# Optimization experiments

Hardware: AMD Instinct MI355X
Metric: run time of the kernel (lower is better)

Reference implementation:

```python
import jax, jax.numpy as jnp
import numpy as np

# dims
B_, L_, DM = 2, 2048, 2048
DS, DC, EXP, HD, NG, CH = 128, 4, 2, 64, 1, 256
DI = EXP * DM                    # d_inner = d_ssm = 4096
NH = DI // HD                    # 64 heads
DIP = 2 * DI + 2 * NG * DS + NH  # 8448 in_proj output
CDIM = DI + 2 * NG * DS          # 4352 conv channels
EPS = 1e-5


def setup_inputs() -> dict:
    key = jax.random.key(0)
    ks = jax.random.split(key, 6)
    u = jax.random.normal(ks[0], (B_, L_, DM), jnp.float32)
    w_in = jax.random.normal(ks[1], (DM, DIP), jnp.float32) * 0.02
    conv_w = jax.random.normal(ks[2], (CDIM, DC), jnp.float32) * (1.0 / np.sqrt(DC))
    conv_b = jnp.zeros((CDIM,), jnp.float32)
    # dt_bias init exactly as the torch module (dt_min=1e-3, dt_max=0.1)
    dt = jnp.exp(jax.random.uniform(ks[3], (NH,)) * (np.log(0.1) - np.log(0.001)) + np.log(0.001))
    dt = jnp.clip(dt, 1e-4)
    dt_bias = dt + jnp.log(-jnp.expm1(-dt))
    A_log = jnp.log(jax.random.uniform(ks[4], (NH,), minval=1.0, maxval=16.0))
    D_skip = jnp.ones((NH,), jnp.float32)
    norm_w = jnp.ones((DI,), jnp.float32)
    return dict(u=u, w_in=w_in, conv_w=conv_w, conv_b=conv_b,
                dt_bias=dt_bias, A_log=A_log, D_skip=D_skip, norm_w=norm_w)


def _segsum(x):
    # x: (..., T) -> (..., T, T) lower-triangular segment sums, -inf above diag
    T = x.shape[-1]
    cs = jnp.cumsum(x, -1)
    ss = cs[..., :, None] - cs[..., None, :]
    return jnp.where(jnp.tril(jnp.ones((T, T), bool)), ss, -jnp.inf)


def _ssd(xdt, dA, Bm, Cm):
    # xdt: (b,l,h,p) = x*dt, dA: (b,l,h) = dt*A, Bm/Cm: (b,l,g,n)
    b, l, h, p = xdt.shape
    c = l // CH
    xr = xdt.reshape(b, c, CH, h, p)
    dAr = dA.reshape(b, c, CH, h).transpose(0, 3, 1, 2)        # (b,h,c,t)
    rep = h // NG
    Bh = jnp.repeat(Bm.reshape(b, c, CH, NG, DS), rep, axis=3)  # (b,c,t,h,n)
    Ch = jnp.repeat(Cm.reshape(b, c, CH, NG, DS), rep, axis=3)
    Acs = jnp.cumsum(dAr, -1)                                   # (b,h,c,t)
    Lm = jnp.exp(_segsum(dAr))                                  # (b,h,c,t,t)
    # intra-chunk (diagonal block) output
    Yd = jnp.einsum('bcthn,bcshn,bhcts,bcshp->bcthp', Ch, Bh, Lm, xr)
    # per-chunk final states
    decay_st = jnp.exp(Acs[..., -1:] - Acs)                     # (b,h,c,t)
    states = jnp.einsum('bcthn,bhct,bcthp->bchpn', Bh, decay_st, xr)
    # inter-chunk recurrence
    pad_last = jnp.pad(Acs[..., -1], ((0, 0), (0, 0), (1, 0)))  # (b,h,c+1)
    dchunk = jnp.exp(_segsum(pad_last))                         # (b,h,c+1,c+1)
    states = jnp.concatenate([jnp.zeros_like(states[:, :1]), states], 1)
    init_st = jnp.einsum('bhzc,bchpn->bzhpn', dchunk, states)[:, :-1]  # (b,c,h,p,n)
    Yo = jnp.einsum('bcthn,bchpn,bhct->bcthp', Ch, init_st, jnp.exp(Acs))
    return (Yd + Yo).reshape(b, l, h, p)


def reference(u, w_in, conv_w, conv_b, dt_bias, A_log, D_skip, norm_w):
    zxbcdt = u @ w_in                           # (b,l,8448)
    z = zxbcdt[..., :DI]
    xBC = zxbcdt[..., DI:DI + CDIM]
    dt = zxbcdt[..., DI + CDIM:]                # (b,l,nheads)
    # causal depthwise conv1d (kernel DC, left pad DC-1) + SiLU
    xp = jnp.pad(xBC, ((0, 0), (DC - 1, 0), (0, 0)))
    xBC = sum(xp[:, k:k + L_, :] * conv_w[:, k] for k in range(DC)) + conv_b
    xBC = jax.nn.silu(xBC)
    x = xBC[..., :DI].reshape(B_, L_, NH, HD)
    Bm = xBC[..., DI:DI + NG * DS].reshape(B_, L_, NG, DS)
    Cm = xBC[..., DI + NG * DS:].reshape(B_, L_, NG, DS)
    dt = jax.nn.softplus(dt + dt_bias)          # dt_softplus=True
    A = -jnp.exp(A_log)
    y = _ssd(x * dt[..., None], dt * A, Bm, Cm)
    y = y + x * D_skip[None, None, :, None]     # D skip, per-head
    y = y.reshape(B_, L_, DI)
    # gated RMSNorm, norm_before_gate=False: rmsnorm(y * silu(z)) * weight
    yg = y * jax.nn.silu(z)
    return yg * jax.lax.rsqrt(jnp.mean(yg * yg, -1, keepdims=True) + EPS) * norm_w
```

## Files before the change

kernel.cpp:

```cpp
#include <hip/hip_runtime.h>
#include <hip/hip_bf16.h>

#define B_SZ   2
#define L_SZ   2048
#define DM     2048
#define DS     128
#define DCV    4
#define HD     64
#define CH     256
#define DI     4096
#define NH     64
#define DIP    8512
#define CDIM   4352
#define NP     8576
#define MROWS  4096
#define NCK    8

typedef __attribute__((ext_vector_type(8))) short bf16x8;
typedef __attribute__((ext_vector_type(4))) float f32x4;
typedef unsigned short u16;

__device__ __forceinline__ u16 f2bf(float f) {
    union { float f; unsigned u; } c; c.f = f;
    unsigned r = c.u + 0x7fffu + ((c.u >> 16) & 1u);
    return (u16)(r >> 16);
}
__device__ __forceinline__ float bf2f(u16 b) {
    union { unsigned u; float f; } c; c.u = ((unsigned)b) << 16; return c.f;
}

__device__ __forceinline__ void async16(const u16* g, u16* l) {
    __builtin_amdgcn_global_load_lds(
        (const __attribute__((address_space(1))) unsigned int*)(g),
        (__attribute__((address_space(3))) unsigned int*)(l),
        16, 0, 0);
}

__global__ void cvt_u_kernel(const float* __restrict__ u, u16* __restrict__ ub) {
    int i = blockIdx.x * 256 + threadIdx.x;
    float4 v = ((const float4*)u)[i];
    ushort4 o;
    o.x = f2bf(v.x); o.y = f2bf(v.y); o.z = f2bf(v.z); o.w = f2bf(v.w);
    ((ushort4*)ub)[i] = o;
}

__global__ void transpose_w_kernel(const float* __restrict__ w, u16* __restrict__ wt) {
    __shared__ float tile[32][33];
    int n0 = blockIdx.x * 32, k0 = blockIdx.y * 32;
    int tx = threadIdx.x & 31, ty = threadIdx.x >> 5;
    for (int j = 0; j < 32; j += 8) {
        int k = k0 + ty + j, n = n0 + tx;
        tile[ty + j][tx] = (n < DIP) ? w[(size_t)k * DIP + n] : 0.f;
    }
    __syncthreads();
    for (int j = 0; j < 32; j += 8) {
        int n = n0 + ty + j, k = k0 + tx;
        wt[(size_t)n * DM + k] = f2bf(tile[tx][ty + j]);
    }
}

#define G_NKT   32
#define G_NBLK  1072
__global__ __launch_bounds__(512) void gemm_kernel(const u16* __restrict__ A,
                                                   const u16* __restrict__ Bt,
                                                   u16* __restrict__ C) {
    __shared__ u16 As[3][256 * 64];
    __shared__ u16 Bs[3][128 * 64];

    int bid = blockIdx.x;
    int bidx = (bid & 7) * (G_NBLK / 8) + (bid >> 3);
    const int width = 8 * 67;
    int group = bidx / width;
    int rem = bidx - group * width;
    int pid_m = group * 8 + (rem & 7);
    int pid_n = rem >> 3;
    const int m0 = pid_m * 256, n0 = pid_n * 128;

    const int tid = threadIdx.x;
    const int lane = tid & 63, wid = tid >> 6;
    const int wm = (wid >> 1) * 64;
    const int wn = (wid & 1) * 64;
    const int quad = lane >> 4, lm = lane & 15;
    const int sx = lm & 7;

    const int srow = tid >> 3;
    const int sc8 = (tid & 7) ^ (srow & 7);
    const u16* aS = A  + (size_t)(m0 + srow) * DM + sc8 * 8;
    const u16* bS = Bt + (size_t)(n0 + srow) * DM + sc8 * 8;
    const int ldo = srow * 64 + (tid & 7) * 8;

    f32x4 acc[4][4] = {};

    for (int t = 0; t < 2; t++) {
        const u16* as = aS + t * 64;
        const u16* bs = bS + t * 64;
        for (int q = 0; q < 4; q++) async16(as + (size_t)q * 64 * DM, &As[t][ldo + q * 4096]);
        for (int q = 0; q < 2; q++) async16(bs + (size_t)q * 64 * DM, &Bs[t][ldo + q * 4096]);
    }
    asm volatile("s_waitcnt vmcnt(6)" ::: "memory");
    __builtin_amdgcn_s_barrier();

    for (int kt = 0; kt < G_NKT; kt++) {
        unsigned cur = (unsigned)kt % 3u;
        unsigned sb  = (unsigned)(kt + 2) % 3u;
        const bool dost = (kt + 2) < G_NKT;
        const u16* ab = &As[cur][0];
        const u16* bb = &Bs[cur][0];
        const u16* as = aS + (kt + 2) * 64;
        const u16* bs = bS + (kt + 2) * 64;

        bf16x8 af[4][2], bf0[2][2];
        for (int i = 0; i < 4; i++) {
            int row = wm + i * 16 + lm;
            for (int ks = 0; ks < 2; ks++)
                af[i][ks] = *(const bf16x8*)(ab + row * 64 + (((ks * 4 + quad) ^ sx) * 8));
        }
        for (int j = 0; j < 2; j++) {
            int row = wn + j * 16 + lm;
            for (int ks = 0; ks < 2; ks++)
                bf0[j][ks] = *(const bf16x8*)(bb + row * 64 + (((ks * 4 + quad) ^ sx) * 8));
        }
        if (dost) {
            async16(as,                   &As[sb][ldo]);
            async16(as + (size_t)64 * DM, &As[sb][ldo + 4096]);
            async16(bs,                   &Bs[sb][ldo]);
        }
        __builtin_amdgcn_s_barrier();
        asm volatile("s_waitcnt lgkmcnt(0)" ::: "memory");
        __builtin_amdgcn_s_setprio(1);
        for (int ks = 0; ks < 2; ks++)
            for (int i = 0; i < 4; i++)
                for (int j = 0; j < 2; j++)
                    acc[i][j] = __builtin_amdgcn_mfma_f32_16x16x32_bf16(af[i][ks], bf0[j][ks], acc[i][j], 0, 0, 0);
        __builtin_amdgcn_s_setprio(0);
        __builtin_amdgcn_s_barrier();

        bf16x8 bf1[2][2];
        for (int j = 0; j < 2; j++) {
            int row = wn + (j + 2) * 16 + lm;
            for (int ks = 0; ks < 2; ks++)
                bf1[j][ks] = *(const bf16x8*)(bb + row * 64 + (((ks * 4 + quad) ^ sx) * 8));
        }
        if (dost) {
            async16(as + (size_t)128 * DM, &As[sb][ldo + 8192]);
            async16(as + (size_t)192 * DM, &As[sb][ldo + 12288]);
            async16(bs + (size_t)64 * DM,  &Bs[sb][ldo + 4096]);
        }
        if (kt < G_NKT - 2) { asm volatile("s_waitcnt vmcnt(6)" ::: "memory"); }
        else                { asm volatile("s_waitcnt vmcnt(0)" ::: "memory"); }
        __builtin_amdgcn_s_barrier();
        asm volatile("s_waitcnt lgkmcnt(0)" ::: "memory");
        __builtin_amdgcn_s_setprio(1);
        for (int ks = 0; ks < 2; ks++)
            for (int i = 0; i < 4; i++)
                for (int j = 0; j < 2; j++)
                    acc[i][j + 2] = __builtin_amdgcn_mfma_f32_16x16x32_bf16(af[i][ks], bf1[j][ks], acc[i][j + 2], 0, 0, 0);
        __builtin_amdgcn_s_setprio(0);
        __builtin_amdgcn_s_barrier();
    }

    for (int i = 0; i < 4; i++)
        for (int j = 0; j < 4; j++)
            for (int r = 0; r < 4; r++) {
                int gm = m0 + wm + i * 16 + quad * 4 + r;
                int gn = n0 + wn + j * 16 + lm;
                C[(size_t)gm * NP + gn] = f2bf(acc[i][j][r]);
            }
}

__global__ void conv_silu_kernel(const u16* __restrict__ zx, const float* __restrict__ cw,
                                 const float* __restrict__ cb, u16* __restrict__ xbc) {
    int c = blockIdx.x * 256 + threadIdx.x;
    int row = blockIdx.y;
    int l = row & (L_SZ - 1);
    float acc = cb[c];
    for (int k = 0; k < DCV; k++) {
        int ls = l - 3 + k;
        if (ls >= 0) acc += bf2f(zx[(size_t)(row - 3 + k) * NP + DI + c]) * cw[c * DCV + k];
    }
    float s = acc / (1.f + expf(-acc));
    xbc[(size_t)row * CDIM + c] = f2bf(s);
}

__global__ void dt_scan_kernel(const u16* __restrict__ zx, const float* __restrict__ dt_bias,
                               const float* __restrict__ A_log, float* __restrict__ dtbT,
                               float* __restrict__ acs) {
    int bid = blockIdx.x;
    int h = bid & 63, c = (bid >> 6) & 7, b = bid >> 9;
    int t = threadIdx.x;
    int row = b * L_SZ + c * CH + t;
    float raw = bf2f(zx[(size_t)row * NP + (DI + CDIM) + h]) + dt_bias[h];
    float dtv = (raw > 20.f) ? raw : log1pf(expf(raw));
    float dA = dtv * (-expf(A_log[h]));
    dtbT[(size_t)h * MROWS + row] = dtv;
    __shared__ float sc[256];
    sc[t] = dA;
    for (int off = 1; off < 256; off <<= 1) {
        __syncthreads();
        float v = (t >= off) ? sc[t - off] : 0.f;
        __syncthreads();
        sc[t] += v;
    }
    acs[((size_t)((b * NH + h) * NCK + c)) * CH + t] = sc[t];
}

__global__ void g_kernel(const u16* __restrict__ xbc, u16* __restrict__ Gb) {
    int blk = blockIdx.x;
    int bc = blk >> 4;
    int tile = blk & 15;
    int tb0 = (tile >> 2) * 64, sb0 = (tile & 3) * 64;
    int row0 = bc * CH;
    __shared__ float Ct[64][65], Bt_[64][65];
    int tq = (threadIdx.x >> 4) * 4;
    int sq = (threadIdx.x & 15) * 4;
    float acc[4][4] = {};
    for (int nh = 0; nh < 2; nh++) {
        __syncthreads();
        int r = threadIdx.x >> 2, cc = (threadIdx.x & 3) * 16;
        for (int q = 0; q < 16; q += 4) {
            ushort4 cv = *(const ushort4*)&xbc[(size_t)(row0 + tb0 + r) * CDIM + (DI + DS) + nh * 64 + cc + q];
            ushort4 bv = *(const ushort4*)&xbc[(size_t)(row0 + sb0 + r) * CDIM + DI + nh * 64 + cc + q];
            Ct[r][cc + q] = bf2f(cv.x); Ct[r][cc + q + 1] = bf2f(cv.y); Ct[r][cc + q + 2] = bf2f(cv.z); Ct[r][cc + q + 3] = bf2f(cv.w);
            Bt_[r][cc + q] = bf2f(bv.x); Bt_[r][cc + q + 1] = bf2f(bv.y); Bt_[r][cc + q + 2] = bf2f(bv.z); Bt_[r][cc + q + 3] = bf2f(bv.w);
        }
        __syncthreads();
        for (int n = 0; n < 64; n++) {
            float a[4], bb[4];
            for (int i = 0; i < 4; i++) a[i] = Ct[tq + i][n];
            for (int j = 0; j < 4; j++) bb[j] = Bt_[sq + j][n];
            for (int i = 0; i < 4; i++)
                for (int j = 0; j < 4; j++) acc[i][j] += a[i] * bb[j];
        }
    }
    for (int i = 0; i < 4; i++)
        for (int j = 0; j < 4; j++) {
            int t = tb0 + tq + i, s = sb0 + sq + j;
            Gb[((size_t)(bc * CH + t)) * CH + s] = (s <= t) ? f2bf(acc[i][j]) : (u16)0;
        }
}

__global__ void bmt_kernel(const u16* __restrict__ xbc, u16* __restrict__ BmT) {
    __shared__ u16 tile[64 * 72];
    int n0 = blockIdx.x * 64, r0 = blockIdx.y * 64;
    int tid = threadIdx.x;
    {
        int r = tid >> 2, seg = (tid & 3) * 16;
        const u16* src = xbc + (size_t)(r0 + r) * CDIM + DI + n0 + seg;
        *(int4*)(tile + r * 72 + seg)     = *(const int4*)(src);
        *(int4*)(tile + r * 72 + seg + 8) = *(const int4*)(src + 8);
    }
    __syncthreads();
    {
        int n = tid >> 2, seg = (tid & 3) * 16;
        union { u16 v[16]; int4 q[2]; } o;
        for (int q = 0; q < 16; q++) o.v[q] = tile[(seg + q) * 72 + n];
        u16* dst = BmT + (size_t)(n0 + n) * MROWS + r0 + seg;
        *(int4*)(dst)     = o.q[0];
        *(int4*)(dst + 8) = o.q[1];
    }
}

__global__ __launch_bounds__(256) void states_kernel(const u16* __restrict__ xbc, const u16* __restrict__ BmT,
                                                     const float* __restrict__ dtbT, const float* __restrict__ acs_g,
                                                     float* __restrict__ states) {
    int bid = blockIdx.x;
    int h = bid & 63, c = (bid >> 6) & 7, b = bid >> 9;
    int row0 = b * L_SZ + c * CH;
    int tid = threadIdx.x;
    int lane = tid & 63, w = tid >> 6;
    int quad = lane >> 4, lm = lane & 15;
    int mh = (w >> 1) * 32, nh = (w & 1) * 64;

    __shared__ float wsc[CH];
    __shared__ u16 XTs[64 * 136];

    {
        size_t abase = ((size_t)((b * NH + h) * NCK + c)) * CH;
        float a255 = acs_g[abase + 255];
        float at = acs_g[abase + tid];
        wsc[tid] = dtbT[(size_t)h * MROWS + row0 + tid] * expf(a255 - at);
    }
    f32x4 acc[2][4] = {};
    for (int k0 = 0; k0 < CH; k0 += 128) {
        __syncthreads();
        {
            int tl = tid >> 1;
            int pseg = (tid & 1) * 32;
            float wv = wsc[k0 + tl];
            const u16* xr = xbc + (size_t)(row0 + k0 + tl) * CDIM + h * HD + pseg;
            for (int q4 = 0; q4 < 4; q4++) {
                bf16x8 v = *(const bf16x8*)(xr + q4 * 8);
                for (int e = 0; e < 8; e++)
                    XTs[(pseg + q4 * 8 + e) * 136 + tl] = f2bf(bf2f((u16)v[e]) * wv);
            }
        }
        __syncthreads();
        for (int ks = 0; ks < 4; ks++) {
            bf16x8 af[2];
            for (int i = 0; i < 2; i++)
                af[i] = *(const bf16x8*)(XTs + (mh + i * 16 + lm) * 136 + ks * 32 + quad * 8);
            for (int j = 0; j < 4; j++) {
                const u16* brow = BmT + (size_t)(nh + j * 16 + lm) * MROWS + row0 + k0 + ks * 32 + quad * 8;
                bf16x8 bfr = *(const bf16x8*)brow;
                for (int i = 0; i < 2; i++)
                    acc[i][j] = __builtin_amdgcn_mfma_f32_16x16x32_bf16(af[i], bfr, acc[i][j], 0, 0, 0);
            }
        }
    }
    float* st = states + (size_t)bid * (HD * DS);
    for (int i = 0; i < 2; i++)
        for (int j = 0; j < 4; j++)
            for (int r = 0; r < 4; r++) {
                int p = mh + i * 16 + quad * 4 + r;
                int n = nh + j * 16 + lm;
                st[p * DS + n] = acc[i][j][r];
            }
}

__global__ void cscan_kernel(float* __restrict__ states, const float* __restrict__ acs_g) {
    int bid = blockIdx.x;
    int h = bid & 63, b = bid >> 6;
    int tid = threadIdx.x;
    float4 carry[8];
    for (int i = 0; i < 8; i++) carry[i] = make_float4(0.f, 0.f, 0.f, 0.f);
    for (int c = 0; c < NCK; c++) {
        size_t base = ((size_t)((b * NCK + c) * NH + h)) * (HD * DS);
        float g = expf(acs_g[((size_t)((b * NH + h) * NCK + c)) * CH + (CH - 1)]);
        float4* sp = (float4*)(states + base);
        for (int i = 0; i < 8; i++) {
            int idx = tid + 256 * i;
            float4 s = sp[idx];
            sp[idx] = carry[i];
            carry[i].x = carry[i].x * g + s.x;
            carry[i].y = carry[i].y * g + s.y;
            carry[i].z = carry[i].z * g + s.z;
            carry[i].w = carry[i].w * g + s.w;
        }
    }
}

__global__ __launch_bounds__(256) void y_kernel(const u16* __restrict__ xbc, const float* __restrict__ dtbT,
                                                const float* __restrict__ acs_g, const u16* __restrict__ Gb,
                                                const float* __restrict__ init_st, const float* __restrict__ D_skip,
                                                u16* __restrict__ y) {
    int bid = blockIdx.x;
    int h = bid & 63, c = (bid >> 6) & 7, b = bid >> 9;
    int bc = b * NCK + c;
    int row0 = b * L_SZ + c * CH;
    int tid = threadIdx.x;
    int lane = tid & 63, w = tid >> 6;
    int wt = w * 64;
    int quad = lane >> 4, lm = lane & 15;

    __shared__ float acs[CH];
    __shared__ u16 Ssb[64 * 136];
    __shared__ u16 XT[64 * 72];

    acs[tid] = acs_g[((size_t)((b * NH + h) * NCK + c)) * CH + tid];
    {
        const float4* sg = (const float4*)(init_st + ((size_t)(bc * NH + h)) * (HD * DS));
        for (int i = 0; i < 8; i++) {
            int g = tid + 256 * i;
            int p = g >> 5, n4 = (g & 31) * 4;
            float4 v = sg[g];
            ushort4 o;
            o.x = f2bf(v.x); o.y = f2bf(v.y); o.z = f2bf(v.z); o.w = f2bf(v.w);
            *(ushort4*)(Ssb + p * 136 + n4) = o;
        }
    }
    __syncthreads();

    f32x4 acc[4][4] = {};
    for (int i = 0; i < 4; i++) {
        const u16* arow = xbc + (size_t)(row0 + wt + i * 16 + lm) * CDIM + (DI + DS);
        for (int ks = 0; ks < 4; ks++) {
            bf16x8 af = *(const bf16x8*)(arow + ks * 32 + quad * 8);
            for (int j = 0; j < 4; j++) {
                bf16x8 bfr = *(const bf16x8*)(Ssb + (j * 16 + lm) * 136 + ks * 32 + quad * 8);
                acc[i][j] = __builtin_amdgcn_mfma_f32_16x16x32_bf16(af, bfr, acc[i][j], 0, 0, 0);
            }
        }
    }
    for (int i = 0; i < 4; i++) {
        float et[4];
        for (int r = 0; r < 4; r++) et[r] = expf(acs[wt + i * 16 + quad * 4 + r]);
        for (int j = 0; j < 4; j++)
            for (int r = 0; r < 4; r++) acc[i][j][r] *= et[r];
    }

    const u16* gball = Gb + (size_t)bc * CH * CH;
    for (int s0 = 0; s0 < CH; s0 += 64) {
        __syncthreads();
        {
            int r = tid >> 2, cseg = (tid & 3) * 16;
            int row = row0 + s0 + r;
            float dv = dtbT[(size_t)h * MROWS + row];
            const u16* xr = xbc + (size_t)row * CDIM + h * HD + cseg;
            for (int q8 = 0; q8 < 2; q8++) {
                bf16x8 v = *(const bf16x8*)(xr + q8 * 8);
                for (int e = 0; e < 8; e++)
                    XT[(cseg + q8 * 8 + e) * 72 + r] = f2bf(bf2f((u16)v[e]) * dv);
            }
        }
        __syncthreads();
        if (wt + 63 < s0) continue;
        for (int i = 0; i < 4; i++) {
            int tTop = wt + i * 16 + 15;
            if (tTop < s0) continue;
            int t = wt + i * 16 + lm;
            float at = acs[t];
            const u16* grow_ = gball + (size_t)t * CH + s0;
            for (int ks = 0; ks < 2; ks++) {
                if (s0 + ks * 32 > tTop) continue;
                bf16x8 g8 = *(const bf16x8*)(grow_ + ks * 32 + quad * 8);
                const float* asp = &acs[s0 + ks * 32 + quad * 8];
                bf16x8 af;
                for (int e = 0; e < 8; e++) {
                    float m = bf2f((u16)g8[e]) * expf(fminf(at - asp[e], 0.f));
                    af[e] = (short)f2bf(m);
                }
                for (int j = 0; j < 4; j++) {
                    bf16x8 bfr = *(const bf16x8*)(XT + (j * 16 + lm) * 72 + ks * 32 + quad * 8);
                    acc[i][j] = __builtin_amdgcn_mfma_f32_16x16x32_bf16(af, bfr, acc[i][j], 0, 0, 0);
                }
            }
        }
    }

    float dsk = D_skip[h];
    for (int i = 0; i < 4; i++)
        for (int r = 0; r < 4; r++) {
            int grow = row0 + wt + i * 16 + quad * 4 + r;
            const u16* xrow = xbc + (size_t)grow * CDIM + h * HD;
            u16* yrow = y + (size_t)grow * DI + h * HD;
            for (int j = 0; j < 4; j++) {
                int p = j * 16 + lm;
                yrow[p] = f2bf(acc[i][j][r] + dsk * bf2f(xrow[p]));
            }
        }
}

__global__ void final_kernel(const u16* __restrict__ y, const u16* __restrict__ zx,
                             const float* __restrict__ norm_w, float* __restrict__ out) {
    int row = blockIdx.x;
    int tid = threadIdx.x;
    __shared__ float red[4];
    float yg[16];
    float ss = 0.f;
    for (int i = 0; i < 16; i++) {
        int col = tid + 256 * i;
        float z = bf2f(zx[(size_t)row * NP + col]);
        float g = bf2f(y[(size_t)row * DI + col]) * (z / (1.f + expf(-z)));
        yg[i] = g; ss += g * g;
    }
    for (int off = 32; off; off >>= 1) ss += __shfl_down(ss, off);
    if ((tid & 63) == 0) red[tid >> 6] = ss;
    __syncthreads();
    if (tid == 0) red[0] = red[0] + red[1] + red[2] + red[3];
    __syncthreads();
    float inv = rsqrtf(red[0] / (float)DI + 1e-5f);
    for (int i = 0; i < 16; i++) {
        int col = tid + 256 * i;
        out[(size_t)row * DI + col] = yg[i] * inv * norm_w[col];
    }
}

extern "C" void kernel_launch(void* const* d_in, const int* in_sizes, int n_in,
                              void* d_out, int out_size, void* d_ws, size_t ws_size,
                              hipStream_t stream) {
    const float* u       = (const float*)d_in[0];
    const float* w_in    = (const float*)d_in[1];
    const float* conv_w  = (const float*)d_in[2];
    const float* conv_b  = (const float*)d_in[3];
    const float* dt_bias = (const float*)d_in[4];
    const float* A_log   = (const float*)d_in[5];
    const float* D_skip  = (const float*)d_in[6];
    const float* norm_w  = (const float*)d_in[7];
    float* out = (float*)d_out;

    const size_t NEEDED = 179306496ull;
    if (ws_size < NEEDED) return;

    char* ws = (char*)d_ws;
    const size_t R = 70254592ull;
    u16*   zx   = (u16*)ws;
    u16*   ubf  = (u16*)(ws + R);
    u16*   wtb  = (u16*)(ws + R + 16777216);
    u16*   xbc  = (u16*)(ws + R);
    float* dtbT = (float*)(ws + R + 35651584);
    float* acs  = (float*)(ws + R + 36700160);
    u16*   Gb   = (u16*)(ws + R + 37748736);
    u16*   BmT  = (u16*)(ws + R + 39845888);
    float* stat = (float*)(ws + R + 41943040);
    u16*   yb   = (u16*)(ws + R + 75497472);

    cvt_u_kernel<<<8192, 256, 0, stream>>>(u, ubf);
    transpose_w_kernel<<<dim3(268, 64), 256, 0, stream>>>(w_in, wtb);
    gemm_kernel<<<G_NBLK, 512, 0, stream>>>(ubf, wtb, zx);
    conv_silu_kernel<<<dim3(17, 4096), 256, 0, stream>>>(zx, conv_w, conv_b, xbc);
    dt_scan_kernel<<<1024, 256, 0, stream>>>(zx, dt_bias, A_log, dtbT, acs);
    g_kernel<<<256, 256, 0, stream>>>(xbc, Gb);
    bmt_kernel<<<dim3(2, 64), 256, 0, stream>>>(xbc, BmT);
    states_kernel<<<1024, 256, 0, stream>>>(xbc, BmT, dtbT, acs, stat);
    cscan_kernel<<<128, 256, 0, stream>>>(stat, acs);
    y_kernel<<<1024, 256, 0, stream>>>(xbc, dtbT, acs, Gb, stat, D_skip, yb);
    final_kernel<<<4096, 256, 0, stream>>>(yb, zx, norm_w, out);
}
```

Measured before the change: 548.2 us.

## Enlarge GEMM tile to 256x256 with BK=32 and vectorize conv and norm kernels

The in_proj GEMM moves from a 256x128 tile to a 256x256 tile with a K-step of 32, so each wave holds 8x4 accumulators and there are half as many blocks. This raises operand reuse per LDS load and cuts redundant A-tile traffic. The weight transpose is padded to 8704 columns, with a bounds guard on the output store. Separately, conv_silu now handles 8 channels per thread with 16-byte loads and stores, and final_kernel uses contiguous vector loads and float4 stores. The costs are higher register pressure, fewer blocks across the CUs, and wasted compute on the padded N columns.

```diff
diff --git a/kernel.cpp b/kernel.cpp
--- a/kernel.cpp
+++ b/kernel.cpp
@@ -13,6 +13,7 @@
 #define DIP    8512
 #define CDIM   4352
 #define NP     8576
+#define NP2    8704
 #define MROWS  4096
 #define NCK    8
 
@@ -59,45 +60,48 @@
     }
 }
 
-#define G_NKT   32
-#define G_NBLK  1072
+#define G_NKT   64
+#define G_NBLK  544
 __global__ __launch_bounds__(512) void gemm_kernel(const u16* __restrict__ A,
                                                    const u16* __restrict__ Bt,
                                                    u16* __restrict__ C) {
-    __shared__ u16 As[3][256 * 64];
-    __shared__ u16 Bs[3][128 * 64];
+    __shared__ u16 As[3][256 * 32];
+    __shared__ u16 Bs[3][256 * 32];
 
     int bid = blockIdx.x;
     int bidx = (bid & 7) * (G_NBLK / 8) + (bid >> 3);
-    const int width = 8 * 67;
+    const int width = 8 * 34;
     int group = bidx / width;
     int rem = bidx - group * width;
     int pid_m = group * 8 + (rem & 7);
     int pid_n = rem >> 3;
-    const int m0 = pid_m * 256, n0 = pid_n * 128;
+    const int m0 = pid_m * 256, n0 = pid_n * 256;
 
     const int tid = threadIdx.x;
-    const int lane = tid & 63, wid = tid >> 6;
-    const int wm = (wid >> 1) * 64;
-    const int wn = (wid & 1) * 64;
+    const int lane = tid & 63;
+    const int wid = tid >> 6;
+    const int wm = (wid >> 2) * 128;
+    const int wn = (wid & 3) * 64;
     const int quad = lane >> 4, lm = lane & 15;
-    const int sx = lm & 7;
-
-    const int srow = tid >> 3;
-    const int sc8 = (tid & 7) ^ (srow & 7);
-    const u16* aS = A  + (size_t)(m0 + srow) * DM + sc8 * 8;
-    const u16* bS = Bt + (size_t)(n0 + srow) * DM + sc8 * 8;
-    const int ldo = srow * 64 + (tid & 7) * 8;
-
-    f32x4 acc[4][4] = {};
+
+    const int srow = tid >> 2;
+    const int c4 = tid & 3;
+    const int scol = (c4 ^ (srow & 3)) * 8;
+    const u16* aS = A  + (size_t)(m0 + srow) * DM + scol;
+    const u16* bS = Bt + (size_t)(n0 + srow) * DM + scol;
+    const int ldo = srow * 32 + c4 * 8;
+
+    f32x4 acc[8][4] = {};
 
     for (int t = 0; t < 2; t++) {
-        const u16* as = aS + t * 64;
-        const u16* bs = bS + t * 64;
-        for (int q = 0; q < 4; q++) async16(as + (size_t)q * 64 * DM, &As[t][ldo + q * 4096]);
-        for (int q = 0; q < 2; q++) async16(bs + (size_t)q * 64 * DM, &Bs[t][ldo + q * 4096]);
-    }
-    asm volatile("s_waitcnt vmcnt(6)" ::: "memory");
+        const u16* as = aS + t * 32;
+        const u16* bs = bS + t * 32;
+        async16(as,                    &As[t][ldo]);
+        async16(as + (size_t)128 * DM, &As[t][ldo + 4096]);
+        async16(bs,                    &Bs[t][ldo]);
+        async16(bs + (size_t)128 * DM, &Bs[t][ldo + 4096]);
+    }
+    asm volatile("s_waitcnt vmcnt(4)" ::: "memory");
     __builtin_amdgcn_s_barrier();
 
     for (int kt = 0; kt < G_NKT; kt++) {
@@ -106,80 +110,99 @@
         const bool dost = (kt + 2) < G_NKT;
         const u16* ab = &As[cur][0];
         const u16* bb = &Bs[cur][0];
-        const u16* as = aS + (kt + 2) * 64;
-        const u16* bs = bS + (kt + 2) * 64;
-
-        bf16x8 af[4][2], bf0[2][2];
+        const u16* as = aS + (kt + 2) * 32;
+        const u16* bs = bS + (kt + 2) * 32;
+
+        bf16x8 af[4], bfr[4];
         for (int i = 0; i < 4; i++) {
             int row = wm + i * 16 + lm;
-            for (int ks = 0; ks < 2; ks++)
-                af[i][ks] = *(const bf16x8*)(ab + row * 64 + (((ks * 4 + quad) ^ sx) * 8));
-        }
-        for (int j = 0; j < 2; j++) {
+            af[i] = *(const bf16x8*)(ab + row * 32 + ((quad ^ (row & 3)) * 8));
+        }
+        for (int j = 0; j < 4; j++) {
             int row = wn + j * 16 + lm;
-            for (int ks = 0; ks < 2; ks++)
-                bf0[j][ks] = *(const bf16x8*)(bb + row * 64 + (((ks * 4 + quad) ^ sx) * 8));
+            bfr[j] = *(const bf16x8*)(bb + row * 32 + ((quad ^ (row & 3)) * 8));
         }
         if (dost) {
-            async16(as,                   &As[sb][ldo]);
-            async16(as + (size_t)64 * DM, &As[sb][ldo + 4096]);
-            async16(bs,                   &Bs[sb][ldo]);
+            async16(as,                    &As[sb][ldo]);
+            async16(as + (size_t)128 * DM, &As[sb][ldo + 4096]);
         }
         __builtin_amdgcn_s_barrier();
         asm volatile("s_waitcnt lgkmcnt(0)" ::: "memory");
         __builtin_amdgcn_s_setprio(1);
-        for (int ks = 0; ks < 2; ks++)
-            for (int i = 0; i < 4; i++)
-                for (int j = 0; j < 2; j++)
-                    acc[i][j] = __builtin_amdgcn_mfma_f32_16x16x32_bf16(af[i][ks], bf0[j][ks], acc[i][j], 0, 0, 0);
+        for (int i = 0; i < 4; i++)
+            for (int j = 0; j < 4; j++)
+                acc[i][j] = __builtin_amdgcn_mfma_f32_16x16x32_bf16(af[i], bfr[j], acc[i][j], 0, 0, 0);
         __builtin_amdgcn_s_setprio(0);
         __builtin_amdgcn_s_barrier();
 
-        bf16x8 bf1[2][2];
-        for (int j = 0; j < 2; j++) {
-            int row = wn + (j + 2) * 16 + lm;
-            for (int ks = 0; ks < 2; ks++)
-                bf1[j][ks] = *(const bf16x8*)(bb + row * 64 + (((ks * 4 + quad) ^ sx) * 8));
+        bf16x8 ag[4];
+        for (int i = 0; i < 4; i++) {
+            int row = wm + 64 + i * 16 + lm;
+            ag[i] = *(const bf16x8*)(ab + row * 32 + ((quad ^ (row & 3)) * 8));
         }
         if (dost) {
-            async16(as + (size_t)128 * DM, &As[sb][ldo + 8192]);
-            async16(as + (size_t)192 * DM, &As[sb][ldo + 12288]);
-            async16(bs + (size_t)64 * DM,  &Bs[sb][ldo + 4096]);
-        }
-        if (kt < G_NKT - 2) { asm volatile("s_waitcnt vmcnt(6)" ::: "memory"); }
+            async16(bs,                    &Bs[sb][ldo]);
+            async16(bs + (size_t)128 * DM, &Bs[sb][ldo + 4096]);
+        }
+        if (kt < G_NKT - 2) { asm volatile("s_waitcnt vmcnt(4)" ::: "memory"); }
         else                { asm volatile("s_waitcnt vmcnt(0)" ::: "memory"); }
         __builtin_amdgcn_s_barrier();
         asm volatile("s_waitcnt lgkmcnt(0)" ::: "memory");
         __builtin_amdgcn_s_setprio(1);
-        for (int ks = 0; ks < 2; ks++)
-            for (int i = 0; i < 4; i++)
-                for (int j = 0; j < 2; j++)
-                    acc[i][j + 2] = __builtin_amdgcn_mfma_f32_16x16x32_bf16(af[i][ks], bf1[j][ks], acc[i][j + 2], 0, 0, 0);
+        for (int i = 0; i < 4; i++)
+            for (int j = 0; j < 4; j++)
+                acc[i + 4][j] = __builtin_amdgcn_mfma_f32_16x16x32_bf16(ag[i], bfr[j], acc[i + 4][j], 0, 0, 0);
         __builtin_amdgcn_s_setprio(0);
         __builtin_amdgcn_s_barrier();
     }
 
-    for (int i = 0; i < 4; i++)
+    for (int i = 0; i < 8; i++)
         for (int j = 0; j < 4; j++)
             for (int r = 0; r < 4; r++) {
                 int gm = m0 + wm + i * 16 + quad * 4 + r;
                 int gn = n0 + wn + j * 16 + lm;
-                C[(size_t)gm * NP + gn] = f2bf(acc[i][j][r]);
+                if (gn < NP)
+                    C[(size_t)gm * NP + gn] = f2bf(acc[i][j][r]);
             }
 }
 
 __global__ void conv_silu_kernel(const u16* __restrict__ zx, const float* __restrict__ cw,
                                  const float* __restrict__ cb, u16* __restrict__ xbc) {
-    int c = blockIdx.x * 256 + threadIdx.x;
-    int row = blockIdx.y;
+    int tid = threadIdx.x;
+    int c8  = blockIdx.x * 32 + (tid & 31);
+    int row = blockIdx.y * 16 + (tid >> 5);
+    int c0  = c8 * 8;
     int l = row & (L_SZ - 1);
-    float acc = cb[c];
+
+    float w_[8][4];
+    {
+        const float4* wp = (const float4*)(cw + (size_t)c0 * 4);
+        for (int e = 0; e < 8; e++) {
+            float4 v = wp[e];
+            w_[e][0] = v.x; w_[e][1] = v.y; w_[e][2] = v.z; w_[e][3] = v.w;
+        }
+    }
+    float acc[8];
+    {
+        float4 b0 = *(const float4*)(cb + c0);
+        float4 b1 = *(const float4*)(cb + c0 + 4);
+        acc[0] = b0.x; acc[1] = b0.y; acc[2] = b0.z; acc[3] = b0.w;
+        acc[4] = b1.x; acc[5] = b1.y; acc[6] = b1.z; acc[7] = b1.w;
+    }
     for (int k = 0; k < DCV; k++) {
         int ls = l - 3 + k;
-        if (ls >= 0) acc += bf2f(zx[(size_t)(row - 3 + k) * NP + DI + c]) * cw[c * DCV + k];
-    }
-    float s = acc / (1.f + expf(-acc));
-    xbc[(size_t)row * CDIM + c] = f2bf(s);
+        if (ls >= 0) {
+            bf16x8 v = *(const bf16x8*)(zx + (size_t)(row - 3 + k) * NP + DI + c0);
+            for (int e = 0; e < 8; e++)
+                acc[e] += bf2f((u16)v[e]) * w_[e][k];
+        }
+    }
+    bf16x8 o;
+    for (int e = 0; e < 8; e++) {
+        float s = acc[e] / (1.f + expf(-acc[e]));
+        o[e] = (short)f2bf(s);
+    }
+    *(bf16x8*)(xbc + (size_t)row * CDIM + c0) = o;
 }
 
 __global__ void dt_scan_kernel(const u16* __restrict__ zx, const float* __restrict__ dt_bias,
@@ -444,14 +467,25 @@
                              const float* __restrict__ norm_w, float* __restrict__ out) {
     int row = blockIdx.x;
     int tid = threadIdx.x;
+    int col0 = tid * 16;
     __shared__ float red[4];
     float yg[16];
     float ss = 0.f;
-    for (int i = 0; i < 16; i++) {
-        int col = tid + 256 * i;
-        float z = bf2f(zx[(size_t)row * NP + col]);
-        float g = bf2f(y[(size_t)row * DI + col]) * (z / (1.f + expf(-z)));
-        yg[i] = g; ss += g * g;
+    {
+        bf16x8 zv0 = *(const bf16x8*)(zx + (size_t)row * NP + col0);
+        bf16x8 zv1 = *(const bf16x8*)(zx + (size_t)row * NP + col0 + 8);
+        bf16x8 yv0 = *(const bf16x8*)(y  + (size_t)row * DI + col0);
+        bf16x8 yv1 = *(const bf16x8*)(y  + (size_t)row * DI + col0 + 8);
+        for (int e = 0; e < 8; e++) {
+            float z = bf2f((u16)zv0[e]);
+            float g = bf2f((u16)yv0[e]) * (z / (1.f + expf(-z)));
+            yg[e] = g; ss += g * g;
+        }
+        for (int e = 0; e < 8; e++) {
+            float z = bf2f((u16)zv1[e]);
+            float g = bf2f((u16)yv1[e]) * (z / (1.f + expf(-z)));
+            yg[8 + e] = g; ss += g * g;
+        }
     }
     for (int off = 32; off; off >>= 1) ss += __shfl_down(ss, off);
     if ((tid & 63) == 0) red[tid >> 6] = ss;
@@ -459,9 +493,14 @@
     if (tid == 0) red[0] = red[0] + red[1] + red[2] + red[3];
     __syncthreads();
     float inv = rsqrtf(red[0] / (float)DI + 1e-5f);
-    for (int i = 0; i < 16; i++) {
-        int col = tid + 256 * i;
-        out[(size_t)row * DI + col] = yg[i] * inv * norm_w[col];
+    for (int q = 0; q < 4; q++) {
+        float4 nw = *(const float4*)(norm_w + col0 + q * 4);
+        float4 o;
+        o.x = yg[q * 4 + 0] * inv * nw.x;
+        o.y = yg[q * 4 + 1] * inv * nw.y;
+        o.z = yg[q * 4 + 2] * inv * nw.z;
+        o.w = yg[q * 4 + 3] * inv * nw.w;
+        *(float4*)(out + (size_t)row * DI + col0 + q * 4) = o;
     }
 }
 
@@ -495,9 +534,9 @@
     u16*   yb   = (u16*)(ws + R + 75497472);
 
     cvt_u_kernel<<<8192, 256, 0, stream>>>(u, ubf);
-    transpose_w_kernel<<<dim3(268, 64), 256, 0, stream>>>(w_in, wtb);
+    transpose_w_kernel<<<dim3(272, 64), 256, 0, stream>>>(w_in, wtb);
     gemm_kernel<<<G_NBLK, 512, 0, stream>>>(ubf, wtb, zx);
-    conv_silu_kernel<<<dim3(17, 4096), 256, 0, stream>>>(zx, conv_w, conv_b, xbc);
+    conv_silu_kernel<<<dim3(17, 256), 512, 0, stream>>>(zx, conv_w, conv_b, xbc);
     dt_scan_kernel<<<1024, 256, 0, stream>>>(zx, dt_bias, A_log, dtbT, acs);
     g_kernel<<<256, 256, 0, stream>>>(xbc, Gb);
     bmt_kernel<<<dim3(2, 64), 256, 0, stream>>>(xbc, BmT);
```

Result: slower. 637.3 us (+16.3%).
